# Performance work log

Hardware: AMD Instinct MI355X
Metric: run time of the kernel (lower is better)

## Reference

```python
import jax, jax.numpy as jnp
import numpy as np

N_NODES = 50000
N_EDGES = 800000
N_GRAPHS = 500
NEG_SLOPE = 0.2
BN_EPS = 1e-5


def gat_layer(x, src, dst, W, al, ar, b):
    # x: [N, F_in]; W: [F_in, H*D]; al/ar: [H, D]; b: [H*D]
    H, D = al.shape
    feat = (x @ W).reshape(N_NODES, H, D)          # [N,H,D]
    el = jnp.sum(feat * al, axis=-1)               # [N,H] src-side score
    er = jnp.sum(feat * ar, axis=-1)               # [N,H] dst-side score
    e = el[src] + er[dst]                          # [E,H]
    e = jnp.where(e > 0, e, NEG_SLOPE * e)         # leaky_relu(0.2)
    # edge softmax over incoming edges of each dst node
    m = jax.ops.segment_max(e, dst, num_segments=N_NODES)       # [N,H]
    ex = jnp.exp(e - m[dst])                                    # [E,H]
    denom = jax.ops.segment_sum(ex, dst, num_segments=N_NODES)  # [N,H]
    alpha = ex / denom[dst]                                     # [E,H]
    # weighted scatter-aggregation of source features
    msg = feat[src] * alpha[:, :, None]                          # [E,H,D]
    out = jax.ops.segment_sum(msg, dst, num_segments=N_NODES)    # [N,H,D]
    return out + b.reshape(H, D)


def batch_norm(x, gamma, beta):
    # training-mode BN over node dimension (biased variance, as torch)
    mu = jnp.mean(x, axis=0)
    var = jnp.mean((x - mu) ** 2, axis=0)
    return gamma * (x - mu) * jax.lax.rsqrt(var + BN_EPS) + beta


def setup_inputs() -> dict:
    key = jax.random.key(0)
    ks = jax.random.split(key, 20)
    s = lambda shape, k, scale=0.05: jax.random.normal(ks[k], shape, jnp.float32) * scale
    return {
        "x": jax.random.normal(ks[0], (N_NODES, 128), jnp.float32),
        "edge_src": jax.random.randint(ks[1], (N_EDGES,), 0, N_NODES),
        "edge_dst": jax.random.randint(ks[2], (N_EDGES,), 0, N_NODES),
        "graph_ids": jax.random.randint(ks[3], (N_NODES,), 0, N_GRAPHS),
        "W0": s((128, 128), 4), "al0": s((4, 32), 5), "ar0": s((4, 32), 6), "b0": jnp.zeros((128,), jnp.float32),
        "W1": s((128, 128), 7), "al1": s((4, 32), 8), "ar1": s((4, 32), 9), "b1": jnp.zeros((128,), jnp.float32),
        "W2": s((128, 32), 10), "al2": s((1, 32), 11), "ar2": s((1, 32), 12), "b2": jnp.zeros((32,), jnp.float32),
        "g0": jnp.ones((128,), jnp.float32), "beta0": jnp.zeros((128,), jnp.float32),
        "g1": jnp.ones((128,), jnp.float32), "beta1": jnp.zeros((128,), jnp.float32),
        "Wc": s((32, 10), 13), "bc": jnp.zeros((10,), jnp.float32),
    }


def reference(x, edge_src, edge_dst, graph_ids,
              W0, al0, ar0, b0, W1, al1, ar1, b1, W2, al2, ar2, b2,
              g0, beta0, g1, beta1, Wc, bc):
    # layer 0: GAT -> flatten heads -> BN -> ReLU (dropout = identity in eval)
    h = gat_layer(x, edge_src, edge_dst, W0, al0, ar0, b0).reshape(N_NODES, -1)
    h = jax.nn.relu(batch_norm(h, g0, beta0))
    # layer 1
    h = gat_layer(h, edge_src, edge_dst, W1, al1, ar1, b1).reshape(N_NODES, -1)
    h = jax.nn.relu(batch_norm(h, g1, beta1))
    # layer 2 (single head) -> squeeze head dim
    h = gat_layer(h, edge_src, edge_dst, W2, al2, ar2, b2)[:, 0, :]  # [N, 32]
    # sum pooling per graph
    hg = jax.ops.segment_sum(h, graph_ids, num_segments=N_GRAPHS)    # [G, 32]
    return hg @ Wc + bc                                              # [G, 10]
```

## Files before the change

### kernel.cpp

```cpp
#include <hip/hip_runtime.h>
#include <math.h>

#define NNODES 50000
#define NEDGES 800000
#define NGRAPHS 500
#define NEG_SLOPE 0.2f
#define BN_EPS 1e-5f
#define NRANGE 196
#define RH_EPB 4096
#define RH_NB ((NEDGES + RH_EPB - 1) / RH_EPB)
#define MAXRE 5120
#define BN_NB 200
#define BN_RPB 250

typedef unsigned int uint;
typedef unsigned short ushort;
typedef __attribute__((ext_vector_type(8))) short bf16x8;
typedef __attribute__((ext_vector_type(4))) float f32x4;

__device__ __forceinline__ float bf2f(ushort u) { return __uint_as_float(((uint)u) << 16); }
__device__ __forceinline__ float bflo(uint u)   { return __uint_as_float(u << 16); }
__device__ __forceinline__ float bfhi(uint u)   { return __uint_as_float(u & 0xffff0000u); }
__device__ __forceinline__ ushort f2bf(float f) {
    uint u = __float_as_uint(f);
    u = (u + 0x7fffu + ((u >> 16) & 1u)) >> 16;
    return (ushort)u;
}

__global__ void prep_kernel(const float* __restrict__ W0, const float* __restrict__ W1,
                            const float* __restrict__ W2, ushort* __restrict__ Wt0,
                            ushort* __restrict__ Wt1, ushort* __restrict__ Wt2,
                            int* __restrict__ rhist) {
    int t = blockIdx.x * 256 + threadIdx.x;
    if (blockIdx.x == 0 && threadIdx.x < NRANGE) rhist[threadIdx.x] = 0;
    if (t < 16384) {
        int k = t >> 7, m = t & 127;
        Wt0[m * 128 + k] = f2bf(W0[t]);
    } else if (t < 32768) {
        int i = t - 16384;
        int k = i >> 7, m = i & 127;
        Wt1[m * 128 + k] = f2bf(W1[i]);
    } else if (t < 36864) {
        int i = t - 32768;
        int k = i >> 5, m = i & 31;
        Wt2[m * 128 + k] = f2bf(W2[i]);
    }
}

__global__ void range_hist_kernel(const int* __restrict__ dst, int* __restrict__ rhist) {
    __shared__ int cnt[NRANGE];
    for (int i = threadIdx.x; i < NRANGE; i += 256) cnt[i] = 0;
    __syncthreads();
    int base = blockIdx.x * RH_EPB;
    int end = base + RH_EPB; if (end > NEDGES) end = NEDGES;
    for (int i = base + threadIdx.x; i < end; i += 256) atomicAdd(&cnt[dst[i] >> 8], 1);
    __syncthreads();
    for (int i = threadIdx.x; i < NRANGE; i += 256)
        if (cnt[i]) atomicAdd(&rhist[i], cnt[i]);
}

__global__ void range_scan_kernel(const int* __restrict__ rhist, int* __restrict__ rbase,
                                  int* __restrict__ rcursor, int* __restrict__ rowptr) {
    __shared__ int ls[256];
    int t = threadIdx.x;
    ls[t] = (t < NRANGE) ? rhist[t] : 0;
    __syncthreads();
    for (int off = 1; off < 256; off <<= 1) {
        int u = (t >= off) ? ls[t - off] : 0;
        __syncthreads();
        ls[t] += u;
        __syncthreads();
    }
    if (t < NRANGE) {
        int b = (t == 0) ? 0 : ls[t - 1];
        rbase[t] = b;
        rcursor[t] = b;
    }
    if (t == 0) { rbase[NRANGE] = NEDGES; rowptr[NNODES] = NEDGES; }
}

__global__ void reorder_kernel(const int* __restrict__ src, const int* __restrict__ dst,
                               int* __restrict__ rcursor, uint* __restrict__ bucket) {
    __shared__ int cnt[NRANGE];
    __shared__ int bofs[NRANGE];
    for (int i = threadIdx.x; i < NRANGE; i += 256) cnt[i] = 0;
    __syncthreads();
    int base = blockIdx.x * RH_EPB;
    int end = base + RH_EPB; if (end > NEDGES) end = NEDGES;
    for (int i = base + threadIdx.x; i < end; i += 256) atomicAdd(&cnt[dst[i] >> 8], 1);
    __syncthreads();
    for (int i = threadIdx.x; i < NRANGE; i += 256) {
        int c = cnt[i];
        bofs[i] = c ? atomicAdd(&rcursor[i], c) : 0;
    }
    __syncthreads();
    for (int i = threadIdx.x; i < NRANGE; i += 256) cnt[i] = 0;
    __syncthreads();
    for (int i = base + threadIdx.x; i < end; i += 256) {
        int d = dst[i], r = d >> 8;
        int loc = atomicAdd(&cnt[r], 1);
        bucket[bofs[r] + loc] = (uint)src[i] | ((uint)(d & 255) << 16);
    }
}

__global__ __launch_bounds__(256) void range_csr_kernel(const int* __restrict__ rbase,
                                                        const uint* __restrict__ bucket,
                                                        int* __restrict__ rowptr,
                                                        int* __restrict__ csr_src) {
    __shared__ uint ebuf[MAXRE];
    __shared__ int deg[256], excl[256], cur[256];
    const int r = blockIdx.x;
    const int b0 = rbase[r];
    const int cnt = rbase[r + 1] - b0;
    const int t = threadIdx.x;
    deg[t] = 0; cur[t] = 0;
    __syncthreads();
    for (int i = t; i < cnt; i += 256) {
        uint e = bucket[b0 + i];
        ebuf[i] = e;
        atomicAdd(&deg[e >> 16], 1);
    }
    __syncthreads();
    excl[t] = deg[t];
    __syncthreads();
    for (int off = 1; off < 256; off <<= 1) {
        int u = (t >= off) ? excl[t - off] : 0;
        __syncthreads();
        excl[t] += u;
        __syncthreads();
    }
    int myExcl = (t == 0) ? 0 : excl[t - 1];
    __syncthreads();
    excl[t] = myExcl;
    __syncthreads();
    int node = r * 256 + t;
    if (node < NNODES) rowptr[node] = b0 + myExcl;
    for (int i = t; i < cnt; i += 256) {
        uint e = ebuf[i];
        int dl = e >> 16;
        int loc = atomicAdd(&cur[dl], 1);
        csr_src[b0 + excl[dl] + loc] = (int)(e & 0xffffu);
    }
}

template <int M, bool HASBN>
__global__ __launch_bounds__(256) void gemm_mfma_kernel(
        const float* __restrict__ X, const ushort* __restrict__ Wt,
        const float* __restrict__ scale, const float* __restrict__ shift,
        const float* __restrict__ al, const float* __restrict__ ar,
        ushort* __restrict__ Y, float* __restrict__ el, float* __restrict__ er, int N) {
    constexpr int H   = M / 32;
    constexpr int BR  = (M == 128) ? 64 : 128;
    constexpr int RT  = (M == 128) ? 4 : 2;
    constexpr int CT  = 2;
    constexpr int LDK = 136;
    __shared__ ushort xs[BR][LDK];
    __shared__ ushort ws[M][LDK];

    const int tid = threadIdx.x, wv = tid >> 6, lane = tid & 63;
    const int rowBase = blockIdx.x * BR;

    for (int i = tid; i < BR * 32; i += 256) {
        int rr = i >> 5, c4 = i & 31;
        int gr = rowBase + rr;
        float4 v = make_float4(0.f, 0.f, 0.f, 0.f);
        if (gr < N) v = *(const float4*)(X + (size_t)gr * 128 + c4 * 4);
        if (HASBN) {
            const float4 sc = *(const float4*)(scale + c4 * 4);
            const float4 sh = *(const float4*)(shift + c4 * 4);
            v.x = fmaxf(v.x * sc.x + sh.x, 0.f);
            v.y = fmaxf(v.y * sc.y + sh.y, 0.f);
            v.z = fmaxf(v.z * sc.z + sh.z, 0.f);
            v.w = fmaxf(v.w * sc.w + sh.w, 0.f);
        }
        ushort* o = &xs[rr][c4 * 4];
        o[0] = f2bf(v.x); o[1] = f2bf(v.y); o[2] = f2bf(v.z); o[3] = f2bf(v.w);
    }
    for (int i = tid; i < M * 16; i += 256) {
        int rr = i >> 4, kc = (i & 15) * 8;
        *(uint4*)&ws[rr][kc] = *(const uint4*)(Wt + rr * 128 + kc);
    }
    __syncthreads();

    const int waveRow = (M == 128) ? 0 : (wv * 32);
    const int waveCol = (M == 128) ? (wv * 32) : 0;
    const int fr = lane & 15, quad = lane >> 4;

    f32x4 acc[RT][CT];
#pragma unroll
    for (int rt = 0; rt < RT; ++rt)
#pragma unroll
        for (int ct = 0; ct < CT; ++ct) acc[rt][ct] = (f32x4){0.f, 0.f, 0.f, 0.f};

#pragma unroll
    for (int ks = 0; ks < 4; ++ks) {
        const int kb = ks * 32 + quad * 8;
        bf16x8 a[RT], b[CT];
#pragma unroll
        for (int rt = 0; rt < RT; ++rt) a[rt] = *(const bf16x8*)&xs[waveRow + rt * 16 + fr][kb];
#pragma unroll
        for (int ct = 0; ct < CT; ++ct) b[ct] = *(const bf16x8*)&ws[waveCol + ct * 16 + fr][kb];
#pragma unroll
        for (int rt = 0; rt < RT; ++rt)
#pragma unroll
            for (int ct = 0; ct < CT; ++ct)
                acc[rt][ct] = __builtin_amdgcn_mfma_f32_16x16x32_bf16(a[rt], b[ct], acc[rt][ct], 0, 0, 0);
    }

#pragma unroll
    for (int rt = 0; rt < RT; ++rt)
#pragma unroll
        for (int ct = 0; ct < CT; ++ct)
#pragma unroll
            for (int rg = 0; rg < 4; ++rg) {
                int gr = rowBase + waveRow + rt * 16 + quad * 4 + rg;
                int gc = waveCol + ct * 16 + fr;
                if (gr < N) Y[(size_t)gr * M + gc] = f2bf(acc[rt][ct][rg]);
            }

    const float a0 = al[waveCol + fr],      a1 = al[waveCol + 16 + fr];
    const float g0 = ar[waveCol + fr],      g1 = ar[waveCol + 16 + fr];
    const int h = (M == 128) ? wv : 0;
#pragma unroll
    for (int rt = 0; rt < RT; ++rt)
#pragma unroll
        for (int rg = 0; rg < 4; ++rg) {
            float pe = acc[rt][0][rg] * a0 + acc[rt][1][rg] * a1;
            float pr = acc[rt][0][rg] * g0 + acc[rt][1][rg] * g1;
#pragma unroll
            for (int off = 1; off < 16; off <<= 1) {
                pe += __shfl_xor(pe, off);
                pr += __shfl_xor(pr, off);
            }
            int grow = rowBase + waveRow + rt * 16 + quad * 4 + rg;
            if (fr == 0 && grow < N) {
                el[grow * H + h] = pe;
                er[grow * H + h] = pr;
            }
        }
}

template <int H>
__global__ void gat_gather_kernel(const int* __restrict__ rowptr, const int* __restrict__ csr_src,
                                  const float* __restrict__ el, const float* __restrict__ er,
                                  const ushort* __restrict__ feat, const float* __restrict__ bias,
                                  float* __restrict__ out) {
    int wave = (blockIdx.x * blockDim.x + threadIdx.x) >> 6;
    int lane = threadIdx.x & 63;
    if (wave >= NNODES) return;
    const int d = wave;
    const int r0 = rowptr[d];
    const int deg = rowptr[d + 1] - r0;

    if constexpr (H == 4) {
        const int h   = lane >> 4;
        const int k   = lane & 15;
        const int grp = lane & 48;
        const int c0  = lane * 2;
        const float erh = er[d * 4 + h];
        float dnm = 0.f, ax = 0.f, ay = 0.f;

        for (int j0 = 0; j0 < deg; j0 += 16) {
            int eidx = j0 + k;
            int s_e = 0;
            float ex = 0.f;
            if (eidx < deg) {
                s_e = csr_src[r0 + eidx];
                float v = el[s_e * 4 + h] + erh;
                v = v > 0.f ? v : NEG_SLOPE * v;
                ex = __expf(v);
            }
            dnm += ex;
            uint u[16];
#pragma unroll
            for (int jj = 0; jj < 16; ++jj) {
                int sj = __builtin_amdgcn_readlane(s_e, jj);
                u[jj] = *(const uint*)(feat + (size_t)sj * 128 + c0);
            }
#pragma unroll
            for (int jj = 0; jj < 16; ++jj) {
                float exj = __shfl(ex, grp + jj);
                ax = fmaf(exj, bflo(u[jj]), ax);
                ay = fmaf(exj, bfhi(u[jj]), ay);
            }
        }
#pragma unroll
        for (int off = 1; off < 16; off <<= 1) dnm += __shfl_xor(dnm, off);
        float inv = (dnm > 0.f) ? 1.f / dnm : 0.f;
        out[(size_t)d * 128 + c0]     = ax * inv + bias[c0];
        out[(size_t)d * 128 + c0 + 1] = ay * inv + bias[c0 + 1];
    } else {
        const int half = lane >> 5;
        const int c    = lane & 31;
        const float erh = er[d];
        float dnm = 0.f, acc = 0.f;

        for (int j0 = 0; j0 < deg; j0 += 32) {
            int eidx = j0 + (lane & 31);
            int s_e = 0;
            float ex = 0.f;
            if (eidx < deg) {
                s_e = csr_src[r0 + eidx];
                float v = el[s_e] + erh;
                v = v > 0.f ? v : NEG_SLOPE * v;
                ex = __expf(v);
            }
            dnm += ex;
            ushort u[16];
#pragma unroll
            for (int jj = 0; jj < 16; ++jj) {
                int sj = __shfl(s_e, 2 * jj + half);
                u[jj] = feat[(size_t)sj * 32 + c];
            }
#pragma unroll
            for (int jj = 0; jj < 16; ++jj) {
                float exj = __shfl(ex, 2 * jj + half);
                acc = fmaf(exj, bf2f(u[jj]), acc);
            }
        }
#pragma unroll
        for (int off = 1; off < 32; off <<= 1) dnm += __shfl_xor(dnm, off);
        acc += __shfl_down(acc, 32);
        if (half == 0) {
            float inv = (dnm > 0.f) ? 1.f / dnm : 0.f;
            out[(size_t)d * 32 + c] = acc * inv + bias[c];
        }
    }
}

__global__ void bn_stats_kernel(const float* __restrict__ X, float* __restrict__ psum,
                                float* __restrict__ psumsq) {
    int c = threadIdx.x & 127;
    int half = threadIdx.x >> 7;
    int r0 = blockIdx.x * BN_RPB;
    float s = 0.f, ss = 0.f;
    for (int r = r0 + half; r < r0 + BN_RPB; r += 2) {
        float v = X[(size_t)r * 128 + c];
        s += v; ss += v * v;
    }
    __shared__ float ls[256], lss[256];
    ls[threadIdx.x] = s;
    lss[threadIdx.x] = ss;
    __syncthreads();
    if (threadIdx.x < 128) {
        psum[blockIdx.x * 128 + c]   = ls[c] + ls[c + 128];
        psumsq[blockIdx.x * 128 + c] = lss[c] + lss[c + 128];
    }
}

__global__ void bn_finalize_kernel(const float* __restrict__ psum, const float* __restrict__ psumsq,
                                   const float* __restrict__ g, const float* __restrict__ beta,
                                   float* __restrict__ scale, float* __restrict__ shift) {
    int c = threadIdx.x;
    float s = 0.f, ss = 0.f;
    for (int b = 0; b < BN_NB; ++b) {
        s += psum[b * 128 + c];
        ss += psumsq[b * 128 + c];
    }
    const float inv = 1.f / NNODES;
    float mu = s * inv;
    float var = ss * inv - mu * mu;
    float sc = g[c] * rsqrtf(var + BN_EPS);
    scale[c] = sc;
    shift[c] = beta[c] - mu * sc;
}

__global__ void pool_kernel(const float* __restrict__ h, const int* __restrict__ gid,
                            float* __restrict__ pooled) {
    int t = blockIdx.x * blockDim.x + threadIdx.x;
    if (t >= NNODES * 32) return;
    int n = t >> 5, c = t & 31;
    atomicAdd(&pooled[gid[n] * 32 + c], h[t]);
}

__global__ void classify_kernel(const float* __restrict__ pooled, const float* __restrict__ Wc,
                                const float* __restrict__ bc, float* __restrict__ out) {
    int t = blockIdx.x * blockDim.x + threadIdx.x;
    if (t >= NGRAPHS * 10) return;
    int gIdx = t / 10, j = t % 10;
    float s = bc[j];
#pragma unroll
    for (int c = 0; c < 32; ++c) s += pooled[gIdx * 32 + c] * Wc[c * 10 + j];
    out[t] = s;
}

extern "C" void kernel_launch(void* const* d_in, const int* in_sizes, int n_in,
                              void* d_out, int out_size, void* d_ws, size_t ws_size,
                              hipStream_t stream) {
    const float* x     = (const float*)d_in[0];
    const int*   esrc  = (const int*)d_in[1];
    const int*   edst  = (const int*)d_in[2];
    const int*   gid   = (const int*)d_in[3];
    const float* W0    = (const float*)d_in[4];
    const float* al0   = (const float*)d_in[5];
    const float* ar0   = (const float*)d_in[6];
    const float* b0    = (const float*)d_in[7];
    const float* W1    = (const float*)d_in[8];
    const float* al1   = (const float*)d_in[9];
    const float* ar1   = (const float*)d_in[10];
    const float* b1    = (const float*)d_in[11];
    const float* W2    = (const float*)d_in[12];
    const float* al2   = (const float*)d_in[13];
    const float* ar2   = (const float*)d_in[14];
    const float* b2    = (const float*)d_in[15];
    const float* g0    = (const float*)d_in[16];
    const float* beta0 = (const float*)d_in[17];
    const float* g1    = (const float*)d_in[18];
    const float* beta1 = (const float*)d_in[19];
    const float* Wc    = (const float*)d_in[20];
    const float* bc    = (const float*)d_in[21];

    float*  bufB   = (float*)d_ws;
    ushort* featbf = (ushort*)(bufB + (size_t)NNODES * 128);
    float*  el     = (float*)(featbf + (size_t)NNODES * 128);
    float*  er     = el + (size_t)NNODES * 4;
    float*  pooled = er + (size_t)NNODES * 4;
    float*  psum   = pooled + NGRAPHS * 32;
    float*  psumsq = psum + BN_NB * 128;
    float*  scale0 = psumsq + BN_NB * 128;
    float*  shift0 = scale0 + 128;
    float*  scale1 = shift0 + 128;
    float*  shift1 = scale1 + 128;
    int* rowptr  = (int*)(shift1 + 128);
    int* csr_src = rowptr + NNODES + 1;
    uint* bucket = (uint*)(csr_src + NEDGES);
    int* rhist   = (int*)(bucket + NEDGES);
    int* rbase   = rhist + NRANGE;
    int* rcursor = rbase + NRANGE + 1;
    ushort* Wt0  = (ushort*)(rcursor + NRANGE);
    ushort* Wt1  = Wt0 + 128 * 128;
    ushort* Wt2  = Wt1 + 128 * 128;

    const int T = 256;
    float* out = (float*)d_out;

    prep_kernel<<<144, T, 0, stream>>>(W0, W1, W2, Wt0, Wt1, Wt2, rhist);

    range_hist_kernel<<<RH_NB, T, 0, stream>>>(edst, rhist);
    range_scan_kernel<<<1, T, 0, stream>>>(rhist, rbase, rcursor, rowptr);
    reorder_kernel<<<RH_NB, T, 0, stream>>>(esrc, edst, rcursor, bucket);
    range_csr_kernel<<<NRANGE, T, 0, stream>>>(rbase, bucket, rowptr, csr_src);

    const int GATHER_BLOCKS  = (NNODES * 64 + T - 1) / T;
    const int GEMM128_BLOCKS = (NNODES + 63) / 64;
    const int GEMM32_BLOCKS  = (NNODES + 127) / 128;
    const int BN_BLOCKS      = BN_NB;

    gemm_mfma_kernel<128, false><<<GEMM128_BLOCKS, T, 0, stream>>>(
        x, Wt0, nullptr, nullptr, al0, ar0, featbf, el, er, NNODES);
    gat_gather_kernel<4><<<GATHER_BLOCKS, T, 0, stream>>>(rowptr, csr_src, el, er, featbf, b0, bufB);
    bn_stats_kernel<<<BN_BLOCKS, T, 0, stream>>>(bufB, psum, psumsq);
    bn_finalize_kernel<<<1, 128, 0, stream>>>(psum, psumsq, g0, beta0, scale0, shift0);

    gemm_mfma_kernel<128, true><<<GEMM128_BLOCKS, T, 0, stream>>>(
        bufB, Wt1, scale0, shift0, al1, ar1, featbf, el, er, NNODES);
    gat_gather_kernel<4><<<GATHER_BLOCKS, T, 0, stream>>>(rowptr, csr_src, el, er, featbf, b1, bufB);
    bn_stats_kernel<<<BN_BLOCKS, T, 0, stream>>>(bufB, psum, psumsq);
    bn_finalize_kernel<<<1, 128, 0, stream>>>(psum, psumsq, g1, beta1, scale1, shift1);

    gemm_mfma_kernel<32, true><<<GEMM32_BLOCKS, T, 0, stream>>>(
        bufB, Wt2, scale1, shift1, al2, ar2, featbf, el, er, NNODES);
    gat_gather_kernel<1><<<GATHER_BLOCKS, T, 0, stream>>>(rowptr, csr_src, el, er, featbf, b2, bufB);

    hipMemsetAsync(pooled, 0, (size_t)NGRAPHS * 32 * 4, stream);
    pool_kernel<<<(NNODES * 32 + T - 1) / T, T, 0, stream>>>(bufB, gid, pooled);
    classify_kernel<<<(NGRAPHS * 10 + T - 1) / T, T, 0, stream>>>(pooled, Wc, bc, out);
}
```

Baseline: 385.1 us.

## Fuse BN stats into gather, BN finalize into GEMM, pooling into last gather

The 4-head gather kernel now loops over several nodes per wave and accumulates per-channel sum and sum-of-squares, then atomically adds them to global accumulators. The separate BN stats and finalize kernels go away, and each GEMM computes scale and shift from those sums at its start. Intermediate activations are stored as bf16 instead of fp32, which halves that traffic. The last gather atomically adds straight into the pooled buffer, which removes the pool kernel. In exchange, float atomics make the BN statistics order-nondeterministic, and the bf16 storage adds rounding before BN.

```diff
diff --git a/kernel.cpp b/kernel.cpp
--- a/kernel.cpp
+++ b/kernel.cpp
@@ -10,8 +10,9 @@
 #define RH_EPB 4096
 #define RH_NB ((NEDGES + RH_EPB - 1) / RH_EPB)
 #define MAXRE 5120
-#define BN_NB 200
-#define BN_RPB 250
+#define G4_REPS 8
+#define G4_NW 6256
+#define G4_NB (G4_NW / 4)
 
 typedef unsigned int uint;
 typedef unsigned short ushort;
@@ -30,9 +31,13 @@
 __global__ void prep_kernel(const float* __restrict__ W0, const float* __restrict__ W1,
                             const float* __restrict__ W2, ushort* __restrict__ Wt0,
                             ushort* __restrict__ Wt1, ushort* __restrict__ Wt2,
-                            int* __restrict__ rhist) {
+                            int* __restrict__ rhist, float* __restrict__ bnacc) {
     int t = blockIdx.x * 256 + threadIdx.x;
     if (blockIdx.x == 0 && threadIdx.x < NRANGE) rhist[threadIdx.x] = 0;
+    if (blockIdx.x == 1) {
+        bnacc[threadIdx.x] = 0.f;
+        bnacc[256 + threadIdx.x] = 0.f;
+    }
     if (t < 16384) {
         int k = t >> 7, m = t & 127;
         Wt0[m * 128 + k] = f2bf(W0[t]);
@@ -145,8 +150,9 @@
 
 template <int M, bool HASBN>
 __global__ __launch_bounds__(256) void gemm_mfma_kernel(
-        const float* __restrict__ X, const ushort* __restrict__ Wt,
-        const float* __restrict__ scale, const float* __restrict__ shift,
+        const void* __restrict__ Xv, const ushort* __restrict__ Wt,
+        const float* __restrict__ gsum, const float* __restrict__ gsumsq,
+        const float* __restrict__ g, const float* __restrict__ beta,
         const float* __restrict__ al, const float* __restrict__ ar,
         ushort* __restrict__ Y, float* __restrict__ el, float* __restrict__ er, int N) {
     constexpr int H   = M / 32;
@@ -156,25 +162,51 @@
     constexpr int LDK = 136;
     __shared__ ushort xs[BR][LDK];
     __shared__ ushort ws[M][LDK];
+    __shared__ float scs[128], shs[128];
 
     const int tid = threadIdx.x, wv = tid >> 6, lane = tid & 63;
     const int rowBase = blockIdx.x * BR;
 
-    for (int i = tid; i < BR * 32; i += 256) {
-        int rr = i >> 5, c4 = i & 31;
-        int gr = rowBase + rr;
-        float4 v = make_float4(0.f, 0.f, 0.f, 0.f);
-        if (gr < N) v = *(const float4*)(X + (size_t)gr * 128 + c4 * 4);
-        if (HASBN) {
-            const float4 sc = *(const float4*)(scale + c4 * 4);
-            const float4 sh = *(const float4*)(shift + c4 * 4);
-            v.x = fmaxf(v.x * sc.x + sh.x, 0.f);
-            v.y = fmaxf(v.y * sc.y + sh.y, 0.f);
-            v.z = fmaxf(v.z * sc.z + sh.z, 0.f);
-            v.w = fmaxf(v.w * sc.w + sh.w, 0.f);
-        }
-        ushort* o = &xs[rr][c4 * 4];
-        o[0] = f2bf(v.x); o[1] = f2bf(v.y); o[2] = f2bf(v.z); o[3] = f2bf(v.w);
+    if (HASBN) {
+        if (tid < 128) {
+            const float inv = 1.f / NNODES;
+            float mu  = gsum[tid] * inv;
+            float var = gsumsq[tid] * inv - mu * mu;
+            float sc  = g[tid] * rsqrtf(var + BN_EPS);
+            scs[tid] = sc;
+            shs[tid] = beta[tid] - mu * sc;
+        }
+        __syncthreads();
+    }
+
+    if (HASBN) {
+        const ushort* X = (const ushort*)Xv;
+        for (int i = tid; i < BR * 16; i += 256) {
+            int rr = i >> 4, q = i & 15;
+            int gr = rowBase + rr;
+            uint4 u = make_uint4(0, 0, 0, 0);
+            if (gr < N) u = *(const uint4*)(X + (size_t)gr * 128 + q * 8);
+            uint arr[4] = {u.x, u.y, u.z, u.w};
+            ushort* o = &xs[rr][q * 8];
+#pragma unroll
+            for (int j = 0; j < 4; ++j) {
+                int c = q * 8 + j * 2;
+                float lo = fmaxf(bflo(arr[j]) * scs[c] + shs[c], 0.f);
+                float hi = fmaxf(bfhi(arr[j]) * scs[c + 1] + shs[c + 1], 0.f);
+                o[j * 2]     = f2bf(lo);
+                o[j * 2 + 1] = f2bf(hi);
+            }
+        }
+    } else {
+        const float* X = (const float*)Xv;
+        for (int i = tid; i < BR * 32; i += 256) {
+            int rr = i >> 5, c4 = i & 31;
+            int gr = rowBase + rr;
+            float4 v = make_float4(0.f, 0.f, 0.f, 0.f);
+            if (gr < N) v = *(const float4*)(X + (size_t)gr * 128 + c4 * 4);
+            ushort* o = &xs[rr][c4 * 4];
+            o[0] = f2bf(v.x); o[1] = f2bf(v.y); o[2] = f2bf(v.z); o[3] = f2bf(v.w);
+        }
     }
     for (int i = tid; i < M * 16; i += 256) {
         int rr = i >> 4, kc = (i & 15) * 8;
@@ -240,23 +272,25 @@
         }
 }
 
-template <int H>
-__global__ void gat_gather_kernel(const int* __restrict__ rowptr, const int* __restrict__ csr_src,
-                                  const float* __restrict__ el, const float* __restrict__ er,
-                                  const ushort* __restrict__ feat, const float* __restrict__ bias,
-                                  float* __restrict__ out) {
-    int wave = (blockIdx.x * blockDim.x + threadIdx.x) >> 6;
-    int lane = threadIdx.x & 63;
-    if (wave >= NNODES) return;
-    const int d = wave;
-    const int r0 = rowptr[d];
-    const int deg = rowptr[d + 1] - r0;
-
-    if constexpr (H == 4) {
-        const int h   = lane >> 4;
-        const int k   = lane & 15;
-        const int grp = lane & 48;
-        const int c0  = lane * 2;
+__global__ __launch_bounds__(256) void gat_gather4_kernel(
+        const int* __restrict__ rowptr, const int* __restrict__ csr_src,
+        const float* __restrict__ el, const float* __restrict__ er,
+        const ushort* __restrict__ feat, const float* __restrict__ bias,
+        ushort* __restrict__ xnext, float* __restrict__ gsum, float* __restrict__ gsumsq) {
+    const int wv = threadIdx.x >> 6, lane = threadIdx.x & 63;
+    const int W = blockIdx.x * 4 + wv;
+    const int h   = lane >> 4;
+    const int k   = lane & 15;
+    const int grp = lane & 48;
+    const int c0  = lane * 2;
+    const float bi0 = bias[c0], bi1 = bias[c0 + 1];
+    float s0 = 0.f, s1 = 0.f, ss0 = 0.f, ss1 = 0.f;
+
+    for (int rep = 0; rep < G4_REPS; ++rep) {
+        const int d = W + rep * G4_NW;
+        if (d >= NNODES) break;
+        const int r0 = rowptr[d];
+        const int deg = rowptr[d + 1] - r0;
         const float erh = er[d * 4 + h];
         float dnm = 0.f, ax = 0.f, ay = 0.f;
 
@@ -287,90 +321,72 @@
 #pragma unroll
         for (int off = 1; off < 16; off <<= 1) dnm += __shfl_xor(dnm, off);
         float inv = (dnm > 0.f) ? 1.f / dnm : 0.f;
-        out[(size_t)d * 128 + c0]     = ax * inv + bias[c0];
-        out[(size_t)d * 128 + c0 + 1] = ay * inv + bias[c0 + 1];
+        float vx = ax * inv + bi0;
+        float vy = ay * inv + bi1;
+        uint pk = ((uint)f2bf(vy) << 16) | (uint)f2bf(vx);
+        *(uint*)(xnext + (size_t)d * 128 + c0) = pk;
+        s0 += vx; ss0 += vx * vx;
+        s1 += vy; ss1 += vy * vy;
+    }
+
+    __shared__ float reds[4][128], redss[4][128];
+    reds[wv][c0] = s0;  reds[wv][c0 + 1] = s1;
+    redss[wv][c0] = ss0; redss[wv][c0 + 1] = ss1;
+    __syncthreads();
+    int t = threadIdx.x;
+    if (t < 128) {
+        atomicAdd(&gsum[t], reds[0][t] + reds[1][t] + reds[2][t] + reds[3][t]);
     } else {
-        const int half = lane >> 5;
-        const int c    = lane & 31;
-        const float erh = er[d];
-        float dnm = 0.f, acc = 0.f;
-
-        for (int j0 = 0; j0 < deg; j0 += 32) {
-            int eidx = j0 + (lane & 31);
-            int s_e = 0;
-            float ex = 0.f;
-            if (eidx < deg) {
-                s_e = csr_src[r0 + eidx];
-                float v = el[s_e] + erh;
-                v = v > 0.f ? v : NEG_SLOPE * v;
-                ex = __expf(v);
-            }
-            dnm += ex;
-            ushort u[16];
-#pragma unroll
-            for (int jj = 0; jj < 16; ++jj) {
-                int sj = __shfl(s_e, 2 * jj + half);
-                u[jj] = feat[(size_t)sj * 32 + c];
-            }
-#pragma unroll
-            for (int jj = 0; jj < 16; ++jj) {
-                float exj = __shfl(ex, 2 * jj + half);
-                acc = fmaf(exj, bf2f(u[jj]), acc);
-            }
-        }
-#pragma unroll
-        for (int off = 1; off < 32; off <<= 1) dnm += __shfl_xor(dnm, off);
-        acc += __shfl_down(acc, 32);
-        if (half == 0) {
-            float inv = (dnm > 0.f) ? 1.f / dnm : 0.f;
-            out[(size_t)d * 32 + c] = acc * inv + bias[c];
-        }
-    }
-}
-
-__global__ void bn_stats_kernel(const float* __restrict__ X, float* __restrict__ psum,
-                                float* __restrict__ psumsq) {
-    int c = threadIdx.x & 127;
-    int half = threadIdx.x >> 7;
-    int r0 = blockIdx.x * BN_RPB;
-    float s = 0.f, ss = 0.f;
-    for (int r = r0 + half; r < r0 + BN_RPB; r += 2) {
-        float v = X[(size_t)r * 128 + c];
-        s += v; ss += v * v;
-    }
-    __shared__ float ls[256], lss[256];
-    ls[threadIdx.x] = s;
-    lss[threadIdx.x] = ss;
-    __syncthreads();
-    if (threadIdx.x < 128) {
-        psum[blockIdx.x * 128 + c]   = ls[c] + ls[c + 128];
-        psumsq[blockIdx.x * 128 + c] = lss[c] + lss[c + 128];
-    }
-}
-
-__global__ void bn_finalize_kernel(const float* __restrict__ psum, const float* __restrict__ psumsq,
-                                   const float* __restrict__ g, const float* __restrict__ beta,
-                                   float* __restrict__ scale, float* __restrict__ shift) {
-    int c = threadIdx.x;
-    float s = 0.f, ss = 0.f;
-    for (int b = 0; b < BN_NB; ++b) {
-        s += psum[b * 128 + c];
-        ss += psumsq[b * 128 + c];
-    }
-    const float inv = 1.f / NNODES;
-    float mu = s * inv;
-    float var = ss * inv - mu * mu;
-    float sc = g[c] * rsqrtf(var + BN_EPS);
-    scale[c] = sc;
-    shift[c] = beta[c] - mu * sc;
-}
-
-__global__ void pool_kernel(const float* __restrict__ h, const int* __restrict__ gid,
-                            float* __restrict__ pooled) {
-    int t = blockIdx.x * blockDim.x + threadIdx.x;
-    if (t >= NNODES * 32) return;
-    int n = t >> 5, c = t & 31;
-    atomicAdd(&pooled[gid[n] * 32 + c], h[t]);
+        int c = t - 128;
+        atomicAdd(&gsumsq[c], redss[0][c] + redss[1][c] + redss[2][c] + redss[3][c]);
+    }
+}
+
+__global__ void gat_gather1_kernel(const int* __restrict__ rowptr, const int* __restrict__ csr_src,
+                                   const float* __restrict__ el, const float* __restrict__ er,
+                                   const ushort* __restrict__ feat, const float* __restrict__ bias,
+                                   const int* __restrict__ gid, float* __restrict__ pooled) {
+    int wave = (blockIdx.x * blockDim.x + threadIdx.x) >> 6;
+    int lane = threadIdx.x & 63;
+    if (wave >= NNODES) return;
+    const int d = wave;
+    const int r0 = rowptr[d];
+    const int deg = rowptr[d + 1] - r0;
+    const int half = lane >> 5;
+    const int c    = lane & 31;
+    const float erh = er[d];
+    float dnm = 0.f, acc = 0.f;
+
+    for (int j0 = 0; j0 < deg; j0 += 32) {
+        int eidx = j0 + (lane & 31);
+        int s_e = 0;
+        float ex = 0.f;
+        if (eidx < deg) {
+            s_e = csr_src[r0 + eidx];
+            float v = el[s_e] + erh;
+            v = v > 0.f ? v : NEG_SLOPE * v;
+            ex = __expf(v);
+        }
+        dnm += ex;
+        ushort u[16];
+#pragma unroll
+        for (int jj = 0; jj < 16; ++jj) {
+            int sj = __shfl(s_e, 2 * jj + half);
+            u[jj] = feat[(size_t)sj * 32 + c];
+        }
+#pragma unroll
+        for (int jj = 0; jj < 16; ++jj) {
+            float exj = __shfl(ex, 2 * jj + half);
+            acc = fmaf(exj, bf2f(u[jj]), acc);
+        }
+    }
+#pragma unroll
+    for (int off = 1; off < 32; off <<= 1) dnm += __shfl_xor(dnm, off);
+    acc += __shfl_down(acc, 32);
+    if (half == 0) {
+        float inv = (dnm > 0.f) ? 1.f / dnm : 0.f;
+        atomicAdd(&pooled[gid[d] * 32 + c], acc * inv + bias[c]);
+    }
 }
 
 __global__ void classify_kernel(const float* __restrict__ pooled, const float* __restrict__ Wc,
@@ -410,18 +426,17 @@
     const float* Wc    = (const float*)d_in[20];
     const float* bc    = (const float*)d_in[21];
 
-    float*  bufB   = (float*)d_ws;
-    ushort* featbf = (ushort*)(bufB + (size_t)NNODES * 128);
-    float*  el     = (float*)(featbf + (size_t)NNODES * 128);
-    float*  er     = el + (size_t)NNODES * 4;
-    float*  pooled = er + (size_t)NNODES * 4;
-    float*  psum   = pooled + NGRAPHS * 32;
-    float*  psumsq = psum + BN_NB * 128;
-    float*  scale0 = psumsq + BN_NB * 128;
-    float*  shift0 = scale0 + 128;
-    float*  scale1 = shift0 + 128;
-    float*  shift1 = scale1 + 128;
-    int* rowptr  = (int*)(shift1 + 128);
+    ushort* featbf  = (ushort*)d_ws;
+    ushort* xnext   = featbf + (size_t)NNODES * 128;
+    float*  el      = (float*)(xnext + (size_t)NNODES * 128);
+    float*  er      = el + (size_t)NNODES * 4;
+    float*  pooled  = er + (size_t)NNODES * 4;
+    float*  bnacc   = pooled + NGRAPHS * 32;
+    float*  gsumA   = bnacc;
+    float*  gsumsqA = bnacc + 128;
+    float*  gsumB   = bnacc + 256;
+    float*  gsumsqB = bnacc + 384;
+    int* rowptr  = (int*)(bnacc + 512);
     int* csr_src = rowptr + NNODES + 1;
     uint* bucket = (uint*)(csr_src + NEDGES);
     int* rhist   = (int*)(bucket + NEDGES);
@@ -434,35 +449,32 @@
     const int T = 256;
     float* out = (float*)d_out;
 
-    prep_kernel<<<144, T, 0, stream>>>(W0, W1, W2, Wt0, Wt1, Wt2, rhist);
+    hipMemsetAsync(pooled, 0, (size_t)NGRAPHS * 32 * 4, stream);
+    prep_kernel<<<144, T, 0, stream>>>(W0, W1, W2, Wt0, Wt1, Wt2, rhist, bnacc);
 
     range_hist_kernel<<<RH_NB, T, 0, stream>>>(edst, rhist);
     range_scan_kernel<<<1, T, 0, stream>>>(rhist, rbase, rcursor, rowptr);
     reorder_kernel<<<RH_NB, T, 0, stream>>>(esrc, edst, rcursor, bucket);
     range_csr_kernel<<<NRANGE, T, 0, stream>>>(rbase, bucket, rowptr, csr_src);
 
-    const int GATHER_BLOCKS  = (NNODES * 64 + T - 1) / T;
+    const int GATHER1_BLOCKS = (NNODES * 64 + T - 1) / T;
     const int GEMM128_BLOCKS = (NNODES + 63) / 64;
     const int GEMM32_BLOCKS  = (NNODES + 127) / 128;
-    const int BN_BLOCKS      = BN_NB;
 
     gemm_mfma_kernel<128, false><<<GEMM128_BLOCKS, T, 0, stream>>>(
-        x, Wt0, nullptr, nullptr, al0, ar0, featbf, el, er, NNODES);
-    gat_gather_kernel<4><<<GATHER_BLOCKS, T, 0, stream>>>(rowptr, csr_src, el, er, featbf, b0, bufB);
-    bn_stats_kernel<<<BN_BLOCKS, T, 0, stream>>>(bufB, psum, psumsq);
-    bn_finalize_kernel<<<1, 128, 0, stream>>>(psum, psumsq, g0, beta0, scale0, shift0);
+        x, Wt0, nullptr, nullptr, nullptr, nullptr, al0, ar0, featbf, el, er, NNODES);
+    gat_gather4_kernel<<<G4_NB, T, 0, stream>>>(rowptr, csr_src, el, er, featbf, b0,
+                                                xnext, gsumA, gsumsqA);
 
     gemm_mfma_kernel<128, true><<<GEMM128_BLOCKS, T, 0, stream>>>(
-        bufB, Wt1, scale0, shift0, al1, ar1, featbf, el, er, NNODES);
-    gat_gather_kernel<4><<<GATHER_BLOCKS, T, 0, stream>>>(rowptr, csr_src, el, er, featbf, b1, bufB);
-    bn_stats_kernel<<<BN_BLOCKS, T, 0, stream>>>(bufB, psum, psumsq);
-    bn_finalize_kernel<<<1, 128, 0, stream>>>(psum, psumsq, g1, beta1, scale1, shift1);
+        xnext, Wt1, gsumA, gsumsqA, g0, beta0, al1, ar1, featbf, el, er, NNODES);
+    gat_gather4_kernel<<<G4_NB, T, 0, stream>>>(rowptr, csr_src, el, er, featbf, b1,
+                                                xnext, gsumB, gsumsqB);
 
     gemm_mfma_kernel<32, true><<<GEMM32_BLOCKS, T, 0, stream>>>(
-        bufB, Wt2, scale1, shift1, al2, ar2, featbf, el, er, NNODES);
-    gat_gather_kernel<1><<<GATHER_BLOCKS, T, 0, stream>>>(rowptr, csr_src, el, er, featbf, b2, bufB);
-
-    hipMemsetAsync(pooled, 0, (size_t)NGRAPHS * 32 * 4, stream);
-    pool_kernel<<<(NNODES * 32 + T - 1) / T, T, 0, stream>>>(bufB, gid, pooled);
+        xnext, Wt2, gsumB, gsumsqB, g1, beta1, al2, ar2, featbf, el, er, NNODES);
+    gat_gather1_kernel<<<GATHER1_BLOCKS, T, 0, stream>>>(rowptr, csr_src, el, er, featbf, b2,
+                                                         gid, pooled);
+
     classify_kernel<<<(NGRAPHS * 10 + T - 1) / T, T, 0, stream>>>(pooled, Wc, bc, out);
 }
```

Result: no change. 381.6 us (-0.9%).
